# Kernel optimization log

Measured on AMD Instinct MI355X. Metric: run time of the kernel, lower is better.

The kernel has to match this reference:

```python
import jax, jax.numpy as jnp
import numpy as np

N = 100000      # nodes
E = 3200000     # edges
H = 64          # node_hidden_dim
DIN = 15        # node_input_dim
DOUT = 12       # output_dim
NT = 5          # num_edge_type
G = 256         # graphs in batch
STEPS = 6       # num_step_prop


def setup_inputs() -> dict:
    key = jax.random.key(0)
    ks = jax.random.split(key, 24)
    s = 0.1
    n = lambda k, shp: jax.random.normal(k, shp, jnp.float32) * s
    return {
        "x": jax.random.normal(ks[0], (N, DIN), jnp.float32),
        "edge_index": jax.random.randint(ks[1], (2, E), 0, N, dtype=jnp.int32),
        "edge_attr": jax.random.randint(ks[2], (E,), 0, NT, dtype=jnp.int32),
        "batch": jnp.sort(jax.random.randint(ks[3], (N,), 0, G, dtype=jnp.int32)),
        "lin0_w": n(ks[4], (DIN, H)), "lin0_b": n(ks[5], (H,)),
        "edge_embed": n(ks[6], (NT, H * H)),
        "conv_bias": n(ks[7], (H,)),
        "gru_w_ih": n(ks[8], (H, 3 * H)), "gru_w_hh": n(ks[9], (H, 3 * H)),
        "gru_b_ih": n(ks[10], (3 * H,)), "gru_b_hh": n(ks[11], (3 * H,)),
        "i_w1": n(ks[12], (2 * H, H)), "i_b1": n(ks[13], (H,)),
        "i_w2": n(ks[14], (H, DOUT)), "i_b2": n(ks[15], (DOUT,)),
        "j_w1": n(ks[16], (H, H)), "j_b1": n(ks[17], (H,)),
        "j_w2": n(ks[18], (H, DOUT)), "j_b2": n(ks[19], (DOUT,)),
    }


def reference(x, edge_index, edge_attr, batch,
              lin0_w, lin0_b, edge_embed, conv_bias,
              gru_w_ih, gru_w_hh, gru_b_ih, gru_b_hh,
              i_w1, i_b1, i_w2, i_b2, j_w1, j_b1, j_w2, j_b2):
    src, dst = edge_index[0], edge_index[1]
    W_types = edge_embed.reshape(NT, H, H)  # per edge-type [H_in, H_out]

    # in-degree for mean aggregation (PyG: isolated nodes get 0)
    deg = jax.ops.segment_sum(jnp.ones((E,), x.dtype), dst, num_segments=N)
    deg = jnp.maximum(deg, 1.0)[:, None]

    out0 = jax.nn.relu(x @ lin0_w + lin0_b)
    out = out0
    h = out0

    for _ in range(STEPS):
        # NNConv: per-edge matmul m_e = x_src[e] @ W[type_e].
        # Only NT=5 edge types exist -> precompute all 5 transforms, then gather.
        T = jnp.einsum('nh,tho->nto', out, W_types)        # [N, NT, H]
        msg = T[src, edge_attr]                            # [E, H] gather
        agg = jax.ops.segment_sum(msg, dst, num_segments=N) / deg + conv_bias
        m = jax.nn.relu(agg)

        # GRU cell (torch gate order: r, z, n)
        gx = m @ gru_w_ih + gru_b_ih
        gh = h @ gru_w_hh + gru_b_hh
        xr, xz, xn = jnp.split(gx, 3, axis=1)
        hr, hz, hn = jnp.split(gh, 3, axis=1)
        r = jax.nn.sigmoid(xr + hr)
        z = jax.nn.sigmoid(xz + hz)
        nn_ = jnp.tanh(xn + r * hn)
        h = (1.0 - z) * nn_ + z * h
        out = h

    # gated readout
    i = jax.nn.sigmoid(
        jax.nn.sigmoid(jnp.concatenate([out, out0], axis=1) @ i_w1 + i_b1) @ i_w2 + i_b2)
    j = jax.nn.sigmoid(out @ j_w1 + j_b1) @ j_w2 + j_b2
    gated = i * j                                          # [N, DOUT]
    return jax.ops.segment_sum(gated, batch, num_segments=G)  # [G, DOUT]
```

## Files before the change

kernel.cpp:

```cpp
#include <hip/hip_runtime.h>
#include <hip/hip_bf16.h>

typedef __hip_bfloat16 bf16;
using short8 = __attribute__((ext_vector_type(8))) short;
using f32x4  = __attribute__((ext_vector_type(4))) float;
using f32x2  = __attribute__((ext_vector_type(2))) float;

#define MFMA16(a,b,c) __builtin_amdgcn_mfma_f32_16x16x32_bf16((a),(b),(c),0,0,0)
#define MAXBUCK 4096
#define SB 72
#define MSTR 72
#define SRCCAP 1024

__device__ __forceinline__ float b2f(bf16 v){ return __bfloat162float(v); }
__device__ __forceinline__ bf16  f2b(float v){ return __float2bfloat16(v); }
__device__ __forceinline__ float sigmf(float x){ return 1.f/(1.f+__expf(-x)); }
__device__ __forceinline__ float tanhfast(float x){
  x = fminf(fmaxf(x,-15.f),15.f);
  float e = __expf(2.f*x);
  return (e-1.f)/(e+1.f);
}
__device__ __forceinline__ short8 ld_frag(const bf16* p){
  return *reinterpret_cast<const short8*>(p);
}
__device__ __forceinline__ float lo16f(unsigned w){
  return __builtin_bit_cast(float, w<<16);
}
__device__ __forceinline__ float hi16f(unsigned w){
  return __builtin_bit_cast(float, w & 0xFFFF0000u);
}
__device__ __forceinline__ short f2bits(float f){
  unsigned u = __builtin_bit_cast(unsigned, f);
  unsigned r = (u + 0x7FFFu + ((u>>16)&1u)) >> 16;
  return (short)r;
}
__device__ __forceinline__ f32x2 up2(unsigned w){
  f32x2 r;
  r.x = __builtin_bit_cast(float, w<<16);
  r.y = __builtin_bit_cast(float, w & 0xFFFF0000u);
  return r;
}
__device__ __forceinline__ f32x2 pk_add(f32x2 a, f32x2 b){
  f32x2 d;
  asm("v_pk_add_f32 %0, %1, %2" : "=v"(d) : "v"(a), "v"(b));
  return d;
}
__device__ __forceinline__ unsigned cvtpk_bf16(float lo, float hi){
  unsigned r;
  asm("v_cvt_pk_bf16_f32 %0, %1, %2" : "=v"(r) : "v"(lo), "v"(hi));
  return r;
}


__global__ void k_sniff(const unsigned int* __restrict__ x, int* __restrict__ flag){
  int t = threadIdx.x;
  int good = 0;
  for (int i=t; i<4096; i+=256){
    unsigned w = x[i];
    unsigned e = (w>>23)&0xFFu;
    unsigned m = w & 0x7FFFFFFFu;
    if ((e>=100u && e<=150u) || m==0u) good++;
  }
  __shared__ int sm[256];
  sm[t]=good; __syncthreads();
  if (t==0){ int s=0; for (int k=0;k<256;k++) s+=sm[k]; *flag = (s>2048)?1:0; }
}

struct PtrPack { const void* p[17]; };

#define CAN_X     0
#define CAN_L0W   1500032
#define CAN_L0B   1500992
#define CAN_EE    1501056
#define CAN_CB    1521536
#define CAN_WIH   1521600
#define CAN_WHH   1533888
#define CAN_BIH   1546176
#define CAN_BHH   1546368
#define CAN_IW1   1546560
#define CAN_IB1   1554752
#define CAN_IW2   1554816
#define CAN_IB2   1555584
#define CAN_JW1   1555648
#define CAN_JB1   1559744
#define CAN_JW2   1559808
#define CAN_JB2   1560576
#define CAN_TOT   1560640

__global__ void k_canon(PtrPack pk, const int* __restrict__ flag, bf16* __restrict__ dst){
  static const int offs[17] = {CAN_X,CAN_L0W,CAN_L0B,CAN_EE,CAN_CB,CAN_WIH,CAN_WHH,
    CAN_BIH,CAN_BHH,CAN_IW1,CAN_IB1,CAN_IW2,CAN_IB2,CAN_JW1,CAN_JB1,CAN_JW2,CAN_JB2};
  static const int szs[17]  = {1500000,960,64,20480,64,12288,12288,192,192,8192,64,768,12,4096,64,768,12};
  int t = blockIdx.x*256+threadIdx.x;
  if (t >= CAN_TOT) return;
  int s = 0;
  #pragma unroll
  for (int k=1;k<17;k++) if (t >= offs[k]) s = k;
  int i = t - offs[s];
  float v = 0.f;
  if (i < szs[s]){
    if (*flag) v = ((const float*)pk.p[s])[i];
    else       v = b2f(((const bf16*)pk.p[s])[i]);
  }
  dst[t] = f2b(v);
}


__global__ __launch_bounds__(1024) void k_scan(const int* __restrict__ cnt, int n,
      int* __restrict__ ptr, int* __restrict__ cursor){
  __shared__ int ws[17];
  int tid = threadIdx.x, lane = tid&63, w = tid>>6;
  int run = 0;
  for (int base=0; base<n; base+=1024){
    int i = base + tid;
    int v = (i<n)? cnt[i] : 0;
    int incl = v;
    #pragma unroll
    for (int off=1; off<64; off<<=1){
      int t = __shfl_up(incl, off, 64);
      if (lane>=off) incl += t;
    }
    if (lane==63) ws[w] = incl;
    __syncthreads();
    if (tid==0){ int r=0; for (int k=0;k<16;k++){ int t=ws[k]; ws[k]=r; r+=t; } ws[16]=r; }
    __syncthreads();
    int excl = run + ws[w] + incl - v;
    if (i<n){
      ptr[i] = excl;
      if (cursor) cursor[i] = excl;
    }
    run += ws[16];
    __syncthreads();
  }
  if (tid==0) ptr[n] = run;
}

__global__ __launch_bounds__(256) void k_bcount(const int* __restrict__ dstv, int E_,
      int nb, int* __restrict__ bkt_cnt){
  __shared__ int lh[MAXBUCK];
  for (int i=threadIdx.x;i<nb;i+=256) lh[i]=0;
  __syncthreads();
  int base = blockIdx.x*4096;
  int end = min(base+4096, E_);
  for (int i=base+threadIdx.x; i<end; i+=256)
    atomicAdd(&lh[dstv[i]>>5], 1);
  __syncthreads();
  for (int i=threadIdx.x;i<nb;i+=256)
    if (lh[i]) atomicAdd(&bkt_cnt[i], lh[i]);
}

__global__ __launch_bounds__(256) void k_bscatter(const int* __restrict__ srcv,
      const int* __restrict__ dstv, const int* __restrict__ eav, int E_, int nb,
      int* __restrict__ cursor, unsigned int* __restrict__ bucketed){
  __shared__ int lh[MAXBUCK];
  __shared__ int lbase[MAXBUCK];
  for (int i=threadIdx.x;i<nb;i+=256) lh[i]=0;
  __syncthreads();
  int base = blockIdx.x*4096;
  int key[16]; int rnk[16]; unsigned pay[16];
  #pragma unroll
  for (int u=0;u<16;u++){
    int i = base + u*256 + threadIdx.x;
    bool valid = i < E_;
    int d = valid? dstv[i] : 0;
    int k = d>>5;
    key[u] = k;
    pay[u] = valid? (((unsigned)((d&31)*5 + eav[i]))<<17) | (unsigned)srcv[i] : 0u;
    rnk[u] = valid? atomicAdd(&lh[k],1) : 0;
  }
  __syncthreads();
  for (int i=threadIdx.x;i<nb;i+=256){
    int c = lh[i];
    lbase[i] = c? atomicAdd(&cursor[i], c) : 0;
  }
  __syncthreads();
  #pragma unroll
  for (int u=0;u<16;u++){
    int i = base + u*256 + threadIdx.x;
    if (i < E_) bucketed[lbase[key[u]] + rnk[u]] = pay[u];
  }
}

__global__ __launch_bounds__(256) void k_bsort(const unsigned int* __restrict__ bucketed,
      const int* __restrict__ bkt_ptr, int nb, int E_,
      int* __restrict__ kptr, int* __restrict__ sorted_src,
      unsigned char* __restrict__ kperm){
  __shared__ int cnt[160], sc[160], cur[160];
  int tid = threadIdx.x;
  int b = blockIdx.x;
  int s = bkt_ptr[b], e = bkt_ptr[b+1];
  if (tid<160) cnt[tid]=0;
  __syncthreads();
  for (int i=s+tid; i<e; i+=256) atomicAdd(&cnt[bucketed[i]>>17], 1);
  __syncthreads();
  if (tid<160) sc[tid]=cnt[tid];
  __syncthreads();
  #pragma unroll
  for (int off=1; off<160; off<<=1){
    int v = 0;
    if (tid<160 && tid>=off) v = sc[tid-off];
    __syncthreads();
    if (tid<160) sc[tid] += v;
    __syncthreads();
  }
  if (tid<160){
    int base = s + sc[tid] - cnt[tid];
    kptr[b*160+tid] = base;
    cur[tid] = base;
  }
  if (b==nb-1 && tid==0) kptr[(size_t)nb*160] = e;
  if (tid<160){
    int hbase = (tid<80)? 0 : 80;
    int me = cnt[tid];
    int r = 0;
    for (int j=0;j<80;j++){
      int jj = hbase+j;
      int cj = cnt[jj];
      r += (cj>me) || (cj==me && jj<tid);
    }
    kperm[((size_t)b*2 + (tid<80?0:1))*80 + r] = (unsigned char)(tid - hbase);
  }
  __syncthreads();
  for (int i=s+tid; i<e; i+=256){
    unsigned p = bucketed[i];
    int pos = atomicAdd(&cur[p>>17], 1);
    sorted_src[pos] = (int)(p & 0x1FFFFu);
  }
}

__global__ __launch_bounds__(256) void k_lin0(const bf16* __restrict__ x,
      const bf16* __restrict__ w, const bf16* __restrict__ b,
      bf16* __restrict__ out0, bf16* __restrict__ h, int N_){
  int idx = blockIdx.x*256+threadIdx.x;
  int n = idx>>6, o = idx&63;
  if (n>=N_) return;
  float acc = b2f(b[o]);
  #pragma unroll
  for (int k=0;k<15;k++) acc += b2f(x[n*15+k]) * b2f(w[k*64+o]);
  bf16 v = f2b(fmaxf(acc,0.f));
  out0[idx]=v; h[idx]=v;
}

__device__ __forceinline__ void d_swz(const unsigned short* src, int KS, int NC,
                                      unsigned short* dst, int nfrag, int t){
  if (t >= nfrag*64) return;
  int lane=t&63, frag=t>>6, cb=frag/KS, ks=frag%KS;
  int c = cb*16 + (lane&15);
  #pragma unroll
  for (int j=0;j<8;j++){
    int k = ks*32 + ((lane>>4)<<3) + j;
    dst[t*8+j] = (c<NC)? src[k*NC+c] : (unsigned short)0;
  }
}

__global__ __launch_bounds__(256) void k_prep(const bf16* __restrict__ ee,
      const bf16* __restrict__ wih, const bf16* __restrict__ whh,
      const bf16* __restrict__ iw1, const bf16* __restrict__ jw1,
      const bf16* __restrict__ iw2, const bf16* __restrict__ jw2,
      unsigned short* __restrict__ wall, unsigned short* __restrict__ wgru,
      unsigned short* __restrict__ wr1, unsigned short* __restrict__ wiw2s,
      unsigned short* __restrict__ wjw2s,
      const int* __restrict__ batch, int N_, int G_, int* __restrict__ gptr){
  int blk = blockIdx.x, tid = threadIdx.x;
  if (blk < 10){
    int t = blk*256+tid;
    if (t<2560){
      int lane=t&63, frag=t>>6, ct=frag/10, ks=frag%10;
      int c = ct*16 + (lane&15);
      #pragma unroll
      for (int j=0;j<8;j++){
        int k = ks*32 + ((lane>>4)<<3) + j;
        int tt = k>>6, kc = k&63;
        wall[t*8+j] = ((const unsigned short*)ee)[tt*4096 + kc*64 + c];
      }
    }
  } else if (blk < 16){
    d_swz((const unsigned short*)wih, 2, 192, wgru, 24, (blk-10)*256+tid);
  } else if (blk < 22){
    d_swz((const unsigned short*)whh, 2, 192, wgru+12288, 24, (blk-16)*256+tid);
  } else if (blk < 26){
    d_swz((const unsigned short*)iw1, 4, 64, wr1, 16, (blk-22)*256+tid);
  } else if (blk < 28){
    d_swz((const unsigned short*)jw1, 2, 64, wr1+8192, 8, (blk-26)*256+tid);
  } else if (blk == 28){
    d_swz((const unsigned short*)iw2, 2, 12, wiw2s, 2, tid);
  } else if (blk == 29){
    d_swz((const unsigned short*)jw2, 2, 12, wjw2s, 2, tid);
  } else {
    int g = (blk-30)*256+tid;
    if (g <= G_){
      int lo=0, hi=N_;
      while (lo<hi){ int mid=(lo+hi)>>1; if (batch[mid] < g) lo=mid+1; else hi=mid; }
      gptr[g]=lo;
    }
  }
}

__global__ __launch_bounds__(256,8) void k_step(const bf16* __restrict__ hin,
      bf16* __restrict__ hout,
      const int* __restrict__ sorted_src, const int* __restrict__ kptr,
      const unsigned char* __restrict__ kperm,
      const unsigned short* __restrict__ wall, const unsigned short* __restrict__ wgru,
      const bf16* __restrict__ conv_bias, const bf16* __restrict__ bih,
      const bf16* __restrict__ bhh, int N_){
  __shared__ unsigned short Sb[80*SB];
  __shared__ int kp[81];
  __shared__ unsigned char pm[80];
  __shared__ char ubuf[SRCCAP*4 + 32];
  int* srcL = (int*)ubuf;
  unsigned short* m_s = (unsigned short*)ubuf;
  int tid=threadIdx.x, lane=tid&63, w=tid>>6;
  int b=blockIdx.x;
  if (tid<81) kp[tid]=kptr[(size_t)b*80+tid];
  if (tid<80) pm[tid]=kperm[(size_t)b*80+tid];
  __syncthreads();
  int s0g = kp[0];
  int elen = kp[80]-s0g;
  int cap = (elen<=SRCCAP)? elen : 0;
  for (int i=tid;i<cap;i+=256) srcL[i]=sorted_src[s0g+i]<<6;
  __syncthreads();
  int g=lane>>3, c=lane&7;
  const bf16* hp = hin + c*8;
  const int sentinel = N_<<6;

  auto run_phase1 = [&](auto GET){
    #pragma unroll 1
    for (int jo=0;jo<5;jo++){
      int pbase = jo*16 + w*4;
      int p  = pm[pbase + (g&3)];
      int p0 = pm[pbase];
      int st = kp[p]-s0g, len = kp[p+1]-kp[p];
      int maxLen = kp[p0+1]-kp[p0];
      int sub = g>>2;
      f32x2 a01={0.f,0.f}, a23={0.f,0.f}, a45={0.f,0.f}, a67={0.f,0.f};
      for (int base=0; base<maxLen; base+=8){
        uint4 hv[4];
        #pragma unroll
        for (int u=0;u<4;u++){
          int idx = base + sub*4 + u;
          int s = GET(st+idx);
          s = (idx < len)? s : sentinel;
          hv[u] = *(const uint4*)(hp + (size_t)s);
        }
        #pragma unroll
        for (int u=0;u<4;u++){
          a01 = pk_add(a01, up2(hv[u].x));
          a23 = pk_add(a23, up2(hv[u].y));
          a45 = pk_add(a45, up2(hv[u].z));
          a67 = pk_add(a67, up2(hv[u].w));
        }
      }
      float a[8] = {a01.x,a01.y,a23.x,a23.y,a45.x,a45.y,a67.x,a67.y};
      #pragma unroll
      for (int j=0;j<8;j++) a[j] += __shfl_xor(a[j], 32);
      if (g<4){
        uint4 v;
        v.x = cvtpk_bf16(a[0],a[1]);
        v.y = cvtpk_bf16(a[2],a[3]);
        v.z = cvtpk_bf16(a[4],a[5]);
        v.w = cvtpk_bf16(a[6],a[7]);
        *reinterpret_cast<uint4*>(&Sb[(size_t)p*SB + c*8]) = v;
      }
    }
  };
  if (cap) run_phase1([&](int rel){ return srcL[rel]; });
  else     run_phase1([&](int rel){ return sorted_src[s0g+rel]<<6; });
  __syncthreads();

  int q=lane>>4, mr=lane&15;
  {
    int ct = w;
    f32x4 acc={0.f,0.f,0.f,0.f};
    #pragma unroll
    for (int ks=0;ks<10;ks++){
      int k0 = ks*32 + q*8;
      int tt = k0>>6, ch = k0&63;
      short8 af = *reinterpret_cast<const short8*>(&Sb[(size_t)(mr*5+tt)*SB + ch]);
      short8 bfrag = *(const short8*)(wall + (size_t)((ct*10+ks)*64+lane)*8);
      acc = MFMA16(af, bfrag, acc);
    }
    int col = ct*16+mr;
    float bi = b2f(conv_bias[col]);
    #pragma unroll
    for (int r=0;r<4;r++){
      int nl = q*4+r;
      int deg = kp[nl*5+5]-kp[nl*5];
      float dv = 1.f/fmaxf((float)deg,1.f);
      m_s[nl*MSTR+col] = (unsigned short)f2bits(fmaxf(acc[r]*dv+bi,0.f));
    }
  }
  __syncthreads();

  {
    int cc = w;
    int na = b*16+mr; if (na>N_-1) na=N_-1;
    short8 am0 = *(const short8*)(&m_s[mr*MSTR + q*8]);
    short8 am1 = *(const short8*)(&m_s[mr*MSTR + 32 + q*8]);
    short8 ah0 = ld_frag(hin + (size_t)na*64 + q*8);
    short8 ah1 = ld_frag(hin + (size_t)na*64 + 32 + q*8);
    const short8* Bw = reinterpret_cast<const short8*>(wgru);
    f32x4 xr={0.f,0.f,0.f,0.f}, xz=xr, xn=xr, hr=xr, hz=xr, hn=xr;
    xr = MFMA16(am0, Bw[((cc  )*2+0)*64+lane], xr);
    xr = MFMA16(am1, Bw[((cc  )*2+1)*64+lane], xr);
    xz = MFMA16(am0, Bw[((cc+4)*2+0)*64+lane], xz);
    xz = MFMA16(am1, Bw[((cc+4)*2+1)*64+lane], xz);
    xn = MFMA16(am0, Bw[((cc+8)*2+0)*64+lane], xn);
    xn = MFMA16(am1, Bw[((cc+8)*2+1)*64+lane], xn);
    hr = MFMA16(ah0, Bw[(24+(cc  )*2+0)*64+lane], hr);
    hr = MFMA16(ah1, Bw[(24+(cc  )*2+1)*64+lane], hr);
    hz = MFMA16(ah0, Bw[(24+(cc+4)*2+0)*64+lane], hz);
    hz = MFMA16(ah1, Bw[(24+(cc+4)*2+1)*64+lane], hz);
    hn = MFMA16(ah0, Bw[(24+(cc+8)*2+0)*64+lane], hn);
    hn = MFMA16(ah1, Bw[(24+(cc+8)*2+1)*64+lane], hn);
    int col = cc*16+mr;
    float bxr=b2f(bih[col]), bxz=b2f(bih[col+64]), bxn=b2f(bih[col+128]);
    float bhr=b2f(bhh[col]), bhz=b2f(bhh[col+64]), bhn=b2f(bhh[col+128]);
    #pragma unroll
    for (int r=0;r<4;r++){
      int row = q*4+r;
      int n = b*16+row;
      if (n < N_){
        float rg = sigmf(xr[r]+bxr + hr[r]+bhr);
        float zg = sigmf(xz[r]+bxz + hz[r]+bhz);
        float ng = tanhfast(xn[r]+bxn + rg*(hn[r]+bhn));
        float ho = b2f(hin[(size_t)n*64+col]);
        hout[(size_t)n*64+col] = f2b((1.f-zg)*ng + zg*ho);
      }
    }
  }
}

__global__ __launch_bounds__(256) void k_read(const bf16* __restrict__ h, const bf16* __restrict__ out0,
      const unsigned short* __restrict__ W, const bf16* __restrict__ ib1, const bf16* __restrict__ jb1,
      const unsigned short* __restrict__ iw2swz, const unsigned short* __restrict__ jw2swz,
      const bf16* __restrict__ ib2, const bf16* __restrict__ jb2,
      float* __restrict__ gated, int N_){
  __shared__ unsigned short lds[12288];
  __shared__ unsigned short sbuf[64*72];
  __shared__ unsigned short tbuf[64*72];
  { const int* s=(const int*)W; int* d=(int*)lds;
    for (int i=threadIdx.x;i<6144;i+=256) d[i]=s[i]; }
  __syncthreads();
  int tid=threadIdx.x, lane=tid&63, w=tid>>6, q=lane>>4;
  int nb = blockIdx.x*64 + w*16;
  int ar = nb + (lane&15); if (ar>N_-1) ar=N_-1;
  short8 ah0 = ld_frag(h + (size_t)ar*64 + q*8),    ah1 = ld_frag(h + (size_t)ar*64 + 32 + q*8);
  short8 ao0 = ld_frag(out0 + (size_t)ar*64 + q*8), ao1 = ld_frag(out0 + (size_t)ar*64 + 32 + q*8);
  const short8* Bi = reinterpret_cast<const short8*>(lds);
  const short8* Bj = reinterpret_cast<const short8*>(lds + 8192);
  int colb = lane&15;
  for (int cb=0; cb<4; cb++){
    f32x4 ai = {0.f,0.f,0.f,0.f};
    ai = MFMA16(ah0, Bi[(cb*4+0)*64+lane], ai);
    ai = MFMA16(ah1, Bi[(cb*4+1)*64+lane], ai);
    ai = MFMA16(ao0, Bi[(cb*4+2)*64+lane], ai);
    ai = MFMA16(ao1, Bi[(cb*4+3)*64+lane], ai);
    f32x4 aj = {0.f,0.f,0.f,0.f};
    aj = MFMA16(ah0, Bj[(cb*2+0)*64+lane], aj);
    aj = MFMA16(ah1, Bj[(cb*2+1)*64+lane], aj);
    int col = cb*16 + colb;
    float bi=b2f(ib1[col]), bj=b2f(jb1[col]);
    #pragma unroll
    for (int r=0;r<4;r++){
      int lrow = w*16 + q*4 + r;
      sbuf[lrow*72+col] = (unsigned short)f2bits(sigmf(ai[r]+bi));
      tbuf[lrow*72+col] = (unsigned short)f2bits(sigmf(aj[r]+bj));
    }
  }
  __syncthreads();
  int mr = lane&15;
  short8 as0 = *(const short8*)(&sbuf[(w*16+mr)*72 + q*8]);
  short8 as1 = *(const short8*)(&sbuf[(w*16+mr)*72 + 32 + q*8]);
  short8 at0 = *(const short8*)(&tbuf[(w*16+mr)*72 + q*8]);
  short8 at1 = *(const short8*)(&tbuf[(w*16+mr)*72 + 32 + q*8]);
  const short8* Bi2 = reinterpret_cast<const short8*>(iw2swz);
  const short8* Bj2 = reinterpret_cast<const short8*>(jw2swz);
  f32x4 ai = {0.f,0.f,0.f,0.f};
  ai = MFMA16(as0, Bi2[lane], ai);
  ai = MFMA16(as1, Bi2[64+lane], ai);
  f32x4 aj = {0.f,0.f,0.f,0.f};
  aj = MFMA16(at0, Bj2[lane], aj);
  aj = MFMA16(at1, Bj2[64+lane], aj);
  int col = lane&15;
  if (col<12){
    float bi=b2f(ib2[col]), bj=b2f(jb2[col]);
    #pragma unroll
    for (int r=0;r<4;r++){
      int row = nb + q*4 + r;
      if (row < N_) gated[(size_t)row*12+col] = sigmf(ai[r]+bi)*(aj[r]+bj);
    }
  }
}

__global__ __launch_bounds__(256) void k_graphsum(const float* __restrict__ gated,
      const int* __restrict__ gptr, const int* __restrict__ flag, void* __restrict__ outp){
  int g = blockIdx.x;
  int s = gptr[g], e = gptr[g+1];
  int tid = threadIdx.x;
  int c = tid & 15, rg = tid >> 4;
  float acc = 0.f;
  if (c < 12)
    for (int row = s + rg; row < e; row += 16) acc += gated[(size_t)row*12 + c];
  __shared__ float sm[256];
  sm[tid] = acc;
  __syncthreads();
  if (rg == 0 && c < 12){
    float t = 0.f;
    for (int k=0;k<16;k++) t += sm[k*16 + c];
    if (*flag) ((float*)outp)[g*12 + c] = t;
    else       ((bf16*) outp)[g*12 + c] = f2b(t);
  }
}


extern "C" void kernel_launch(void* const* d_in, const int* in_sizes, int n_in,
                              void* d_out, int out_size, void* d_ws, size_t ws_size,
                              hipStream_t stream){
  const int*  ei    = (const int*) d_in[1];
  const int*  ea    = (const int*) d_in[2];
  const int*  batch = (const int*) d_in[3];

  const int N_ = in_sizes[3];
  const int E_ = in_sizes[2];
  const int G_ = out_size / 12;
  const int nb  = (N_ + 31) >> 5;
  const int nbs = (N_ + 15) >> 4;

  char* ws = (char*)d_ws;
  size_t off = 0;
  auto alloc = [&](size_t bytes)->size_t{
    size_t o = off; off += (bytes + 255) & ~(size_t)255; return o;
  };

  size_t oOut0   = alloc((size_t)N_*64*2);
  size_t oH0     = alloc((size_t)(N_+1)*64*2);
  size_t oH1     = alloc((size_t)(N_+1)*64*2);
  size_t oGated  = alloc((size_t)N_*12*4);
  size_t oBEdges = alloc((size_t)E_*4);
  size_t oSorted = alloc((size_t)E_*4 + 256);
  size_t oKptr   = alloc(((size_t)nb*160+2)*4);
  size_t oKperm  = alloc((size_t)nb*160);
  size_t oCanon  = alloc((size_t)CAN_TOT*2);
  size_t oCnt    = alloc((size_t)nb*4);
  size_t oBPtr   = alloc((size_t)(nb+1)*4);
  size_t oBCur   = alloc((size_t)nb*4);
  size_t oGptr   = alloc((size_t)(G_+1)*4);
  size_t oFlag   = alloc(256);
  size_t oWall   = alloc((size_t)20480*2);
  size_t oWgru   = alloc((size_t)24576*2);
  size_t oWr1    = alloc((size_t)12288*2);
  size_t oWiw2   = alloc((size_t)1024*2);
  size_t oWjw2   = alloc((size_t)1024*2);

  bf16*  out0    = (bf16*)(ws + oOut0);
  bf16*  h0      = (bf16*)(ws + oH0);
  bf16*  h1      = (bf16*)(ws + oH1);
  float* gated   = (float*)(ws + oGated);
  unsigned int* bucketed = (unsigned int*)(ws + oBEdges);
  int*   sorted_src = (int*)(ws + oSorted);
  int*   kptr    = (int*)(ws + oKptr);
  unsigned char* kperm = (unsigned char*)(ws + oKperm);
  bf16*  can     = (bf16*)(ws + oCanon);
  int*   bkt_cnt = (int*)(ws + oCnt);
  int*   bkt_ptr = (int*)(ws + oBPtr);
  int*   bkt_cur = (int*)(ws + oBCur);
  int*   gptr    = (int*)(ws + oGptr);
  int*   flag    = (int*)(ws + oFlag);
  unsigned short* wall  = (unsigned short*)(ws + oWall);
  unsigned short* wgru  = (unsigned short*)(ws + oWgru);
  unsigned short* wr1   = (unsigned short*)(ws + oWr1);
  unsigned short* wiw2s = (unsigned short*)(ws + oWiw2);
  unsigned short* wjw2s = (unsigned short*)(ws + oWjw2);

  const bf16* xC    = can + CAN_X;
  const bf16* l0wC  = can + CAN_L0W;
  const bf16* l0bC  = can + CAN_L0B;
  const bf16* eeC   = can + CAN_EE;
  const bf16* cbC   = can + CAN_CB;
  const bf16* wihC  = can + CAN_WIH;
  const bf16* whhC  = can + CAN_WHH;
  const bf16* bihC  = can + CAN_BIH;
  const bf16* bhhC  = can + CAN_BHH;
  const bf16* iw1C  = can + CAN_IW1;
  const bf16* ib1C  = can + CAN_IB1;
  const bf16* iw2C  = can + CAN_IW2;
  const bf16* ib2C  = can + CAN_IB2;
  const bf16* jw1C  = can + CAN_JW1;
  const bf16* jb1C  = can + CAN_JB1;
  const bf16* jw2C  = can + CAN_JW2;
  const bf16* jb2C  = can + CAN_JB2;

  PtrPack pk;
  pk.p[0]=d_in[0];  pk.p[1]=d_in[4];  pk.p[2]=d_in[5];  pk.p[3]=d_in[6];
  pk.p[4]=d_in[7];  pk.p[5]=d_in[8];  pk.p[6]=d_in[9];  pk.p[7]=d_in[10];
  pk.p[8]=d_in[11]; pk.p[9]=d_in[12]; pk.p[10]=d_in[13]; pk.p[11]=d_in[14];
  pk.p[12]=d_in[15]; pk.p[13]=d_in[16]; pk.p[14]=d_in[17]; pk.p[15]=d_in[18];
  pk.p[16]=d_in[19];

  const int gNw  = (N_+63)/64;
  const int gEc  = (E_+4095)/4096;

  k_sniff<<<1, 256, 0, stream>>>((const unsigned int*)d_in[0], flag);
  k_canon<<<(CAN_TOT+255)/256, 256, 0, stream>>>(pk, flag, can);
  hipMemsetAsync(ws + oCnt, 0, (size_t)nb*4, stream);
  hipMemsetAsync(ws + oH0 + (size_t)N_*128, 0, 128, stream);
  hipMemsetAsync(ws + oH1 + (size_t)N_*128, 0, 128, stream);
  k_bcount<<<gEc, 256, 0, stream>>>(ei + E_, E_, nb, bkt_cnt);
  k_scan<<<1, 1024, 0, stream>>>(bkt_cnt, nb, bkt_ptr, bkt_cur);
  k_bscatter<<<gEc, 256, 0, stream>>>(ei, ei + E_, ea, E_, nb, bkt_cur, bucketed);
  k_bsort<<<nb, 256, 0, stream>>>(bucketed, bkt_ptr, nb, E_, kptr, sorted_src, kperm);
  k_lin0<<<(N_*64+255)/256, 256, 0, stream>>>(xC, l0wC, l0bC, out0, h0, N_);
  k_prep<<<32, 256, 0, stream>>>(eeC, wihC, whhC, iw1C, jw1C, iw2C, jw2C,
                                 wall, wgru, wr1, wiw2s, wjw2s, batch, N_, G_, gptr);

  bf16* hb[2] = {h0, h1};
  for (int step = 0; step < 6; ++step){
    k_step<<<nbs, 256, 0, stream>>>(hb[step&1], hb[(step+1)&1], sorted_src, kptr, kperm,
                                    wall, wgru, cbC, bihC, bhhC, N_);
  }
  bf16* hfin = hb[0];

  k_read<<<gNw, 256, 0, stream>>>(hfin, out0, wr1, ib1C, jb1C, wiw2s, wjw2s,
                                  ib2C, jb2C, gated, N_);
  k_graphsum<<<G_, 256, 0, stream>>>(gated, gptr, flag, d_out);
}
```

Measured before the change: 701.9 us.

## Software-pipeline phase-1 neighbor gathers across segments with double buffering

```diff
diff --git a/kernel.cpp b/kernel.cpp
--- a/kernel.cpp
+++ b/kernel.cpp
@@ -22,12 +22,6 @@
 }
 __device__ __forceinline__ short8 ld_frag(const bf16* p){
   return *reinterpret_cast<const short8*>(p);
-}
-__device__ __forceinline__ float lo16f(unsigned w){
-  return __builtin_bit_cast(float, w<<16);
-}
-__device__ __forceinline__ float hi16f(unsigned w){
-  return __builtin_bit_cast(float, w & 0xFFFF0000u);
 }
 __device__ __forceinline__ short f2bits(float f){
   unsigned u = __builtin_bit_cast(unsigned, f);
@@ -317,37 +311,69 @@
   int s0g = kp[0];
   int elen = kp[80]-s0g;
   int cap = (elen<=SRCCAP)? elen : 0;
-  for (int i=tid;i<cap;i+=256) srcL[i]=sorted_src[s0g+i]<<6;
+  for (int i=tid;i<cap;i+=256) srcL[i]=sorted_src[s0g+i]<<7;
   __syncthreads();
   int g=lane>>3, c=lane&7;
-  const bf16* hp = hin + c*8;
-  const int sentinel = N_<<6;
+  const int cOff = c<<4;
+  const int sub4 = (g>>2)*4;
+  const int pmk  = w*4 + (g&3);
+  const int pm0  = w*4;
+  const int sentB = N_<<7;
+  const char* hbase = (const char*)hin;
 
   auto run_phase1 = [&](auto GET){
-    #pragma unroll 1
-    for (int jo=0;jo<5;jo++){
-      int pbase = jo*16 + w*4;
-      int p  = pm[pbase + (g&3)];
-      int p0 = pm[pbase];
-      int st = kp[p]-s0g, len = kp[p+1]-kp[p];
-      int maxLen = kp[p0+1]-kp[p0];
-      int sub = g>>2;
+    int pC, stC, lenC, maxC;
+    auto params = [&](int jo){
+      int pp = pm[jo*16 + pmk];
+      int p0 = pm[jo*16 + pm0];
+      pC = pp;
+      int k0 = kp[pp];
+      stC  = k0 - s0g;
+      lenC = kp[pp+1] - k0;
+      maxC = kp[p0+1] - kp[p0];
+    };
+    uint4 A[4], B[4];
+    auto issue = [&](uint4* buf, int st_, int base, int len_){
+      #pragma unroll
+      for (int u=0;u<4;u++){
+        int idx = base + sub4 + u;
+        int s = GET(st_ + idx);
+        s = (idx < len_)? s : sentB;
+        buf[u] = *(const uint4*)(hbase + (unsigned)(s + cOff));
+      }
+    };
+    auto body = [&](int jo, uint4* cur, uint4* nxt){
+      int pS=pC, stS=stC, lenS=lenC, maxS=maxC;
+      uint4 T[4];
+      bool has2 = 8 < maxS;
+      if (has2) issue(T, stS, 8, lenS);
+      if (jo<4){ params(jo+1); issue(nxt, stC, 0, lenC); }
       f32x2 a01={0.f,0.f}, a23={0.f,0.f}, a45={0.f,0.f}, a67={0.f,0.f};
-      for (int base=0; base<maxLen; base+=8){
-        uint4 hv[4];
+      #pragma unroll
+      for (int u=0;u<4;u++){
+        a01 = pk_add(a01, up2(cur[u].x));
+        a23 = pk_add(a23, up2(cur[u].y));
+        a45 = pk_add(a45, up2(cur[u].z));
+        a67 = pk_add(a67, up2(cur[u].w));
+      }
+      if (has2){
         #pragma unroll
         for (int u=0;u<4;u++){
-          int idx = base + sub*4 + u;
-          int s = GET(st+idx);
-          s = (idx < len)? s : sentinel;
-          hv[u] = *(const uint4*)(hp + (size_t)s);
+          a01 = pk_add(a01, up2(T[u].x));
+          a23 = pk_add(a23, up2(T[u].y));
+          a45 = pk_add(a45, up2(T[u].z));
+          a67 = pk_add(a67, up2(T[u].w));
         }
-        #pragma unroll
-        for (int u=0;u<4;u++){
-          a01 = pk_add(a01, up2(hv[u].x));
-          a23 = pk_add(a23, up2(hv[u].y));
-          a45 = pk_add(a45, up2(hv[u].z));
-          a67 = pk_add(a67, up2(hv[u].w));
+        #pragma unroll 1
+        for (int bse=16; bse<maxS; bse+=8){
+          issue(T, stS, bse, lenS);
+          #pragma unroll
+          for (int u=0;u<4;u++){
+            a01 = pk_add(a01, up2(T[u].x));
+            a23 = pk_add(a23, up2(T[u].y));
+            a45 = pk_add(a45, up2(T[u].z));
+            a67 = pk_add(a67, up2(T[u].w));
+          }
         }
       }
       float a[8] = {a01.x,a01.y,a23.x,a23.y,a45.x,a45.y,a67.x,a67.y};
@@ -359,12 +385,19 @@
         v.y = cvtpk_bf16(a[2],a[3]);
         v.z = cvtpk_bf16(a[4],a[5]);
         v.w = cvtpk_bf16(a[6],a[7]);
-        *reinterpret_cast<uint4*>(&Sb[(size_t)p*SB + c*8]) = v;
+        *reinterpret_cast<uint4*>(&Sb[(size_t)pS*SB + c*8]) = v;
       }
-    }
+    };
+    params(0);
+    issue(A, stC, 0, lenC);
+    body(0, A, B);
+    body(1, B, A);
+    body(2, A, B);
+    body(3, B, A);
+    body(4, A, B);
   };
   if (cap) run_phase1([&](int rel){ return srcL[rel]; });
-  else     run_phase1([&](int rel){ return sorted_src[s0g+rel]<<6; });
+  else     run_phase1([&](int rel){ return sorted_src[s0g+rel]<<7; });
   __syncthreads();
 
   int q=lane>>4, mr=lane&15;
```

Result: slower. 1.062 ms (+51.3%).

## Replace global bucket scatter with per-chunk local sort and segmented gather

Applied to the files above, without the earlier changes.

```diff
diff --git a/kernel.cpp b/kernel.cpp
--- a/kernel.cpp
+++ b/kernel.cpp
@@ -11,6 +11,8 @@
 #define SB 72
 #define MSTR 72
 #define SRCCAP 1024
+#define CHK 8192
+#define BCAP 2816
 
 __device__ __forceinline__ float b2f(bf16 v){ return __bfloat162float(v); }
 __device__ __forceinline__ bf16  f2b(float v){ return __float2bfloat16(v); }
@@ -22,12 +24,6 @@
 }
 __device__ __forceinline__ short8 ld_frag(const bf16* p){
   return *reinterpret_cast<const short8*>(p);
-}
-__device__ __forceinline__ float lo16f(unsigned w){
-  return __builtin_bit_cast(float, w<<16);
-}
-__device__ __forceinline__ float hi16f(unsigned w){
-  return __builtin_bit_cast(float, w & 0xFFFF0000u);
 }
 __device__ __forceinline__ short f2bits(float f){
   unsigned u = __builtin_bit_cast(unsigned, f);
@@ -135,63 +131,93 @@
   if (tid==0) ptr[n] = run;
 }
 
-__global__ __launch_bounds__(256) void k_bcount(const int* __restrict__ dstv, int E_,
-      int nb, int* __restrict__ bkt_cnt){
+__global__ __launch_bounds__(512) void k_csort(const int* __restrict__ srcv,
+      const int* __restrict__ dstv, const int* __restrict__ eav, int E_, int nb, int NC,
+      unsigned int* __restrict__ bucketed, int* __restrict__ rs, int* __restrict__ bkt_cnt){
   __shared__ int lh[MAXBUCK];
-  for (int i=threadIdx.x;i<nb;i+=256) lh[i]=0;
-  __syncthreads();
-  int base = blockIdx.x*4096;
-  int end = min(base+4096, E_);
-  for (int i=base+threadIdx.x; i<end; i+=256)
-    atomicAdd(&lh[dstv[i]>>5], 1);
-  __syncthreads();
-  for (int i=threadIdx.x;i<nb;i+=256)
-    if (lh[i]) atomicAdd(&bkt_cnt[i], lh[i]);
-}
-
-__global__ __launch_bounds__(256) void k_bscatter(const int* __restrict__ srcv,
-      const int* __restrict__ dstv, const int* __restrict__ eav, int E_, int nb,
-      int* __restrict__ cursor, unsigned int* __restrict__ bucketed){
-  __shared__ int lh[MAXBUCK];
-  __shared__ int lbase[MAXBUCK];
-  for (int i=threadIdx.x;i<nb;i+=256) lh[i]=0;
-  __syncthreads();
-  int base = blockIdx.x*4096;
-  int key[16]; int rnk[16]; unsigned pay[16];
-  #pragma unroll
-  for (int u=0;u<16;u++){
-    int i = base + u*256 + threadIdx.x;
-    bool valid = i < E_;
-    int d = valid? dstv[i] : 0;
-    int k = d>>5;
-    key[u] = k;
-    pay[u] = valid? (((unsigned)((d&31)*5 + eav[i]))<<17) | (unsigned)srcv[i] : 0u;
-    rnk[u] = valid? atomicAdd(&lh[k],1) : 0;
-  }
-  __syncthreads();
-  for (int i=threadIdx.x;i<nb;i+=256){
-    int c = lh[i];
-    lbase[i] = c? atomicAdd(&cursor[i], c) : 0;
-  }
-  __syncthreads();
-  #pragma unroll
-  for (int u=0;u<16;u++){
-    int i = base + u*256 + threadIdx.x;
-    if (i < E_) bucketed[lbase[key[u]] + rnk[u]] = pay[u];
-  }
-}
-
-__global__ __launch_bounds__(256) void k_bsort(const unsigned int* __restrict__ bucketed,
+  __shared__ int lofs[MAXBUCK];
+  __shared__ int ws[9];
+  int c = blockIdx.x, tid = threadIdx.x;
+  int base = c*CHK, end = min(base+CHK, E_);
+  for (int i=tid;i<nb;i+=512) lh[i]=0;
+  __syncthreads();
+  for (int i=base+tid; i<end; i+=512) atomicAdd(&lh[dstv[i]>>5], 1);
+  __syncthreads();
+  int lane=tid&63, w=tid>>6;
+  int run=0;
+  for (int bb=0; bb<nb; bb+=512){
+    int i=bb+tid;
+    int v=(i<nb)? lh[i]:0;
+    int incl=v;
+    #pragma unroll
+    for (int off=1;off<64;off<<=1){
+      int t=__shfl_up(incl,off,64);
+      if (lane>=off) incl+=t;
+    }
+    if (lane==63) ws[w]=incl;
+    __syncthreads();
+    if (tid==0){ int r=0; for(int k=0;k<8;k++){int t=ws[k];ws[k]=r;r+=t;} ws[8]=r; }
+    __syncthreads();
+    if (i<nb) lofs[i]= run + ws[w] + incl - v;
+    run += ws[8];
+    __syncthreads();
+  }
+  for (int i=tid;i<nb;i+=512){
+    rs[(size_t)i*NC + c] = base + lofs[i];
+    int cntv = lh[i];
+    if (cntv) atomicAdd(&bkt_cnt[i], cntv);
+  }
+  if (tid==0) rs[(size_t)nb*NC + c] = end;
+  __syncthreads();
+  for (int i=base+tid;i<end;i+=512){
+    int d = dstv[i];
+    int bin = d>>5;
+    int pos = base + atomicAdd(&lofs[bin], 1);
+    bucketed[pos] = (((unsigned)((d&31)*5 + eav[i]))<<17) | (unsigned)srcv[i];
+  }
+}
+
+__global__ __launch_bounds__(256) void k_bsort2(const unsigned int* __restrict__ bucketed,
+      const int* __restrict__ rs, int NC,
       const int* __restrict__ bkt_ptr, int nb, int E_,
       int* __restrict__ kptr, int* __restrict__ sorted_src,
       unsigned char* __restrict__ kperm){
+  __shared__ unsigned sbuf[BCAP];
+  __shared__ int rofs[1025];
   __shared__ int cnt[160], sc[160], cur[160];
-  int tid = threadIdx.x;
-  int b = blockIdx.x;
+  int b = blockIdx.x, tid = threadIdx.x;
   int s = bkt_ptr[b], e = bkt_ptr[b+1];
+  int size = e - s;
+  const int* rowA = rs + (size_t)b*NC;
+  const int* rowB = rs + (size_t)(b+1)*NC;
+  for (int c2=tid; c2<NC; c2+=256) rofs[c2] = rowB[c2] - rowA[c2];
+  __syncthreads();
+  if (tid==0){
+    int acc=0;
+    for (int c2=0;c2<NC;c2++){ int t=rofs[c2]; rofs[c2]=acc; acc+=t; }
+    rofs[NC]=acc;
+  }
+  __syncthreads();
+  bool staged = (size <= BCAP);
+  if (staged){
+    for (int c2=tid; c2<NC; c2+=256){
+      int st = rowA[c2];
+      int ln = rowB[c2] - st;
+      int d0 = rofs[c2];
+      for (int k=0;k<ln;k++) sbuf[d0+k] = bucketed[st+k];
+    }
+  }
+  __syncthreads();
   if (tid<160) cnt[tid]=0;
   __syncthreads();
-  for (int i=s+tid; i<e; i+=256) atomicAdd(&cnt[bucketed[i]>>17], 1);
+  if (staged){
+    for (int i=tid;i<size;i+=256) atomicAdd(&cnt[sbuf[i]>>17], 1);
+  } else {
+    for (int c2=0;c2<NC;c2++){
+      int st=rowA[c2], ln=rowB[c2]-st;
+      for (int k=tid;k<ln;k+=256) atomicAdd(&cnt[bucketed[st+k]>>17], 1);
+    }
+  }
   __syncthreads();
   if (tid<160) sc[tid]=cnt[tid];
   __syncthreads();
@@ -204,9 +230,9 @@
     __syncthreads();
   }
   if (tid<160){
-    int base = s + sc[tid] - cnt[tid];
-    kptr[b*160+tid] = base;
-    cur[tid] = base;
+    int basek = s + sc[tid] - cnt[tid];
+    kptr[b*160+tid] = basek;
+    cur[tid] = basek;
   }
   if (b==nb-1 && tid==0) kptr[(size_t)nb*160] = e;
   if (tid<160){
@@ -221,10 +247,21 @@
     kperm[((size_t)b*2 + (tid<80?0:1))*80 + r] = (unsigned char)(tid - hbase);
   }
   __syncthreads();
-  for (int i=s+tid; i<e; i+=256){
-    unsigned p = bucketed[i];
-    int pos = atomicAdd(&cur[p>>17], 1);
-    sorted_src[pos] = (int)(p & 0x1FFFFu);
+  if (staged){
+    for (int i=tid;i<size;i+=256){
+      unsigned p = sbuf[i];
+      int pos = atomicAdd(&cur[p>>17], 1);
+      sorted_src[pos] = (int)(p & 0x1FFFFu);
+    }
+  } else {
+    for (int c2=0;c2<NC;c2++){
+      int st=rowA[c2], ln=rowB[c2]-st;
+      for (int k=tid;k<ln;k+=256){
+        unsigned p = bucketed[st+k];
+        int pos = atomicAdd(&cur[p>>17], 1);
+        sorted_src[pos] = (int)(p & 0x1FFFFu);
+      }
+    }
   }
 }
 
@@ -321,7 +358,7 @@
   __syncthreads();
   int g=lane>>3, c=lane&7;
   const bf16* hp = hin + c*8;
-  const int sentinel = N_<<6;
+  const int sent = N_<<6;
 
   auto run_phase1 = [&](auto GET){
     #pragma unroll 1
@@ -339,7 +376,7 @@
         for (int u=0;u<4;u++){
           int idx = base + sub*4 + u;
           int s = GET(st+idx);
-          s = (idx < len)? s : sentinel;
+          s = (idx < len)? s : sent;
           hv[u] = *(const uint4*)(hp + (size_t)s);
         }
         #pragma unroll
@@ -525,6 +562,7 @@
   const int G_ = out_size / 12;
   const int nb  = (N_ + 31) >> 5;
   const int nbs = (N_ + 15) >> 4;
+  const int NC  = (E_ + CHK - 1) / CHK;
 
   char* ws = (char*)d_ws;
   size_t off = 0;
@@ -538,12 +576,12 @@
   size_t oGated  = alloc((size_t)N_*12*4);
   size_t oBEdges = alloc((size_t)E_*4);
   size_t oSorted = alloc((size_t)E_*4 + 256);
+  size_t oRS     = alloc((size_t)(nb+1)*NC*4);
   size_t oKptr   = alloc(((size_t)nb*160+2)*4);
   size_t oKperm  = alloc((size_t)nb*160);
   size_t oCanon  = alloc((size_t)CAN_TOT*2);
   size_t oCnt    = alloc((size_t)nb*4);
   size_t oBPtr   = alloc((size_t)(nb+1)*4);
-  size_t oBCur   = alloc((size_t)nb*4);
   size_t oGptr   = alloc((size_t)(G_+1)*4);
   size_t oFlag   = alloc(256);
   size_t oWall   = alloc((size_t)20480*2);
@@ -558,12 +596,12 @@
   float* gated   = (float*)(ws + oGated);
   unsigned int* bucketed = (unsigned int*)(ws + oBEdges);
   int*   sorted_src = (int*)(ws + oSorted);
+  int*   rs      = (int*)(ws + oRS);
   int*   kptr    = (int*)(ws + oKptr);
   unsigned char* kperm = (unsigned char*)(ws + oKperm);
   bf16*  can     = (bf16*)(ws + oCanon);
   int*   bkt_cnt = (int*)(ws + oCnt);
   int*   bkt_ptr = (int*)(ws + oBPtr);
-  int*   bkt_cur = (int*)(ws + oBCur);
   int*   gptr    = (int*)(ws + oGptr);
   int*   flag    = (int*)(ws + oFlag);
   unsigned short* wall  = (unsigned short*)(ws + oWall);
@@ -598,17 +636,15 @@
   pk.p[16]=d_in[19];
 
   const int gNw  = (N_+63)/64;
-  const int gEc  = (E_+4095)/4096;
 
   k_sniff<<<1, 256, 0, stream>>>((const unsigned int*)d_in[0], flag);
   k_canon<<<(CAN_TOT+255)/256, 256, 0, stream>>>(pk, flag, can);
   hipMemsetAsync(ws + oCnt, 0, (size_t)nb*4, stream);
   hipMemsetAsync(ws + oH0 + (size_t)N_*128, 0, 128, stream);
   hipMemsetAsync(ws + oH1 + (size_t)N_*128, 0, 128, stream);
-  k_bcount<<<gEc, 256, 0, stream>>>(ei + E_, E_, nb, bkt_cnt);
-  k_scan<<<1, 1024, 0, stream>>>(bkt_cnt, nb, bkt_ptr, bkt_cur);
-  k_bscatter<<<gEc, 256, 0, stream>>>(ei, ei + E_, ea, E_, nb, bkt_cur, bucketed);
-  k_bsort<<<nb, 256, 0, stream>>>(bucketed, bkt_ptr, nb, E_, kptr, sorted_src, kperm);
+  k_csort<<<NC, 512, 0, stream>>>(ei, ei + E_, ea, E_, nb, NC, bucketed, rs, bkt_cnt);
+  k_scan<<<1, 1024, 0, stream>>>(bkt_cnt, nb, bkt_ptr, nullptr);
+  k_bsort2<<<nb, 256, 0, stream>>>(bucketed, rs, NC, bkt_ptr, nb, E_, kptr, sorted_src, kperm);
   k_lin0<<<(N_*64+255)/256, 256, 0, stream>>>(xC, l0wC, l0bC, out0, h0, N_);
   k_prep<<<32, 256, 0, stream>>>(eeC, wihC, whhC, iw1C, jw1C, iw2C, jw2C,
                                  wall, wgru, wr1, wiw2s, wjw2s, batch, N_, G_, gptr);
```

Result: no change. 690.9 us (-1.6%).
